# Optimization experiments

Hardware: AMD Instinct MI355X
Metric: run time of the kernel (lower is better)

## Reference

```python
import jax, jax.numpy as jnp
import numpy as np

IMG_SIZE = 416.0
CLASS_NUM = 80
NUM_ANCH = 3
MAX_GT = 64  # fixed padding for per-image valid GT boxes (original uses a variable-size python loop)


def _bce_logits(x, t):
    # BCEWithLogits, elementwise: softplus(x) - x*t  (numerically stable)
    return jax.nn.softplus(x) - x * t


def _make_noobj_mask(pred_boxes, targets):
    # pred_boxes: [B,G,G,3,4] in pixel units; targets: [B,G,G,3,85]
    B, G = pred_boxes.shape[0], pred_boxes.shape[1]
    N = G * G * NUM_ANCH
    conf = targets[..., 4].reshape(B, N)
    boxes = targets[..., 0:4].reshape(B, N, 4)
    # gather up to MAX_GT ground-truth boxes per image (conf>0 are the valid ones)
    top_conf, idx = jax.lax.top_k(conf, MAX_GT)            # [B,M]
    gt = jnp.take_along_axis(boxes, idx[..., None], axis=1)  # [B,M,4]
    valid = top_conf > 0.0                                   # [B,M]

    p = pred_boxes.reshape(B, N, 4)
    pxy = p[:, :, None, 0:2]   # [B,N,1,2]
    pwh = p[:, :, None, 2:4]
    gxy = gt[:, None, :, 0:2]  # [B,1,M,2]
    gwh = gt[:, None, :, 2:4]

    imin = jnp.maximum(pxy - pwh / 2, gxy - gwh / 2)
    imax = jnp.minimum(pxy + pwh / 2, gxy + gwh / 2)
    iwh = jnp.maximum(imax - imin, 0.0)
    inter = iwh[..., 0] * iwh[..., 1]                        # [B,N,M]
    area_p = pwh[..., 0] * pwh[..., 1]
    area_g = gwh[..., 0] * gwh[..., 1]
    iou = inter / (area_p + area_g - inter + 1e-9)
    iou = jnp.where(valid[:, None, :], iou, 0.0)
    best_iou = jnp.max(iou, axis=-1)                         # [B,N]
    noobj = (best_iou < 0.6).astype(pred_boxes.dtype)
    return noobj.reshape(B, G, G, NUM_ANCH)


def reference(preds, targets, anchors):
    B, G = preds.shape[0], preds.shape[1]
    ratio = IMG_SIZE / G
    p = preds.reshape(B, G, G, NUM_ANCH, 5 + CLASS_NUM)
    box_xy_raw, box_wh_raw, conf_logit, cls_logit = jnp.split(p, [2, 4, 5], axis=-1)

    # grid offsets: offset[i,j] = (j, i)
    gx, gy = jnp.meshgrid(jnp.arange(G, dtype=preds.dtype), jnp.arange(G, dtype=preds.dtype))
    offset = jnp.stack([gx, gy], axis=-1).reshape(G, G, 1, 2)

    sig_xy = jax.nn.sigmoid(box_xy_raw)
    box_xy = (sig_xy + offset) * ratio                 # pixel units
    box_wh = jnp.exp(box_wh_raw) * anchors             # (anchors/ratio)*ratio = anchors
    pred_boxes = jnp.concatenate([box_xy, box_wh], axis=-1)

    preds_xy = box_xy / ratio - offset                 # == sig_xy
    true_xy = targets[..., 0:2] / ratio - offset
    true_wh = targets[..., 2:4] / anchors
    preds_wh = box_wh / anchors
    true_wh = jnp.where(true_wh == 0.0, 1.0, true_wh)
    preds_wh = jnp.where(preds_wh == 0.0, 1.0, preds_wh)
    true_wh = jnp.log(jnp.clip(true_wh, 1e-9, 1e9))
    preds_wh = jnp.log(jnp.clip(preds_wh, 1e-9, 1e9))

    obj = (targets[..., 4] > 0.0).astype(preds.dtype)  # [B,G,G,3]
    obj_e = obj[..., None]
    scale = 2.0 - targets[..., 2:3] / IMG_SIZE * targets[..., 3:4] / IMG_SIZE  # [B,G,G,3,1]

    txty_loss = jnp.sum(obj_e * (preds_xy - true_xy) ** 2 * scale) / B
    twth_loss = jnp.sum(obj_e * (preds_wh - true_wh) ** 2 * scale) / B

    noobj = _make_noobj_mask(pred_boxes, targets)      # [B,G,G,3]
    noobj_conf_mask = (1.0 - obj) * noobj
    conf_t = targets[..., 4:5]
    noobj_conf_loss = jnp.sum(noobj_conf_mask[..., None] * _bce_logits(conf_logit, conf_t)) / B
    obj_conf_loss = jnp.sum(obj_e * _bce_logits(conf_logit, conf_t)) / B
    class_loss = jnp.sum(obj_e * _bce_logits(cls_logit, targets[..., 5:])) / B

    total_loss = txty_loss + twth_loss + noobj_conf_loss + obj_conf_loss + class_loss
    return (txty_loss, twth_loss, noobj_conf_loss, obj_conf_loss, class_loss, total_loss)


def setup_inputs() -> dict:
    key = jax.random.key(0)
    ks = jax.random.split(key, 5)
    B, G, A, C = 32, 52, NUM_ANCH, CLASS_NUM
    N = G * G * A
    M_OBJ = 40  # GT boxes per image (< MAX_GT)
    preds = jax.random.normal(ks[0], (B, G, G, A * (5 + C)), jnp.float32) * 0.5
    idx = jax.random.randint(ks[1], (B, M_OBJ), 0, N)
    xy = jax.random.uniform(ks[2], (B, M_OBJ, 2), jnp.float32, 0.0, IMG_SIZE)
    wh = jax.random.uniform(ks[3], (B, M_OBJ, 2), jnp.float32, 16.0, 128.0)
    cid = jax.random.randint(ks[4], (B, M_OBJ), 0, C)
    onehot = jax.nn.one_hot(cid, C, dtype=jnp.float32)
    vals = jnp.concatenate([xy, wh, jnp.ones((B, M_OBJ, 1), jnp.float32), onehot], axis=-1)
    t = jnp.zeros((B, N, 5 + C), jnp.float32)
    t = t.at[jnp.arange(B)[:, None], idx].set(vals)
    targets = t.reshape(B, G, G, A, 5 + C)
    anchors = jnp.array([[10.0, 13.0], [16.0, 30.0], [33.0, 23.0]], jnp.float32)
    return {"preds": preds, "targets": targets, "anchors": anchors}
```

## Files before the change

kernel.cpp:

```cpp
#include <hip/hip_runtime.h>
#include <math.h>

#define GSZ 52
#define NA 3
#define NCLS 80
#define CH 85
#define NCA (GSZ*GSZ*NA)
#define MAXGT 64
#define MCHUNK 32
#define CLSU 16

__device__ __forceinline__ float softplus_fast(float x) {
    return fmaxf(x, 0.0f) + __logf(1.0f + __expf(-fabsf(x)));
}

__global__ void k_init(int* cnt, int B) {
    if (threadIdx.x < B) cnt[threadIdx.x] = 0;
}

__device__ __forceinline__ void emit_gt(const float* __restrict__ tg, int glob,
                                        int* cnt, float4* __restrict__ gtbox,
                                        int2* __restrict__ gtinfo) {
    const float* r = tg + (size_t)glob * CH;
    int b    = glob / NCA;
    int nloc = glob - b * NCA;
    int cid = 0;
#pragma unroll 16
    for (int c = 0; c < NCLS; c++) if (r[5 + c] > 0.5f) cid = c;
    int pos = atomicAdd(cnt + b, 1);
    if (pos < MAXGT) {
        gtbox[b * MAXGT + pos]  = make_float4(r[0], r[1], r[2], r[3]);
        gtinfo[b * MAXGT + pos] = make_int2(nloc, cid);
    }
}

__global__ __launch_bounds__(256) void k_scan(
    const float* __restrict__ tg, const float* __restrict__ pr,
    const float* __restrict__ anchors, int nrec, int* cnt,
    float4* __restrict__ gtbox, int2* __restrict__ gtinfo,
    float4* __restrict__ boxdec, float* __restrict__ confdec) {
    int tid = threadIdx.x;
    int rec = blockIdx.x * 128 + (tid & 127);
    if (rec >= nrec) return;

    const float* rp = pr + (size_t)rec * CH;
    if (tid < 128) {
        float r0 = rp[0], r1 = rp[1], r2 = rp[2], r3 = rp[3];
        int b    = rec / NCA;
        int n    = rec - b * NCA;
        int a    = n % NA;
        int cell = n / NA;
        int gi = cell / GSZ, gj = cell % GSZ;
        float aw = anchors[2 * a], ah = anchors[2 * a + 1];
        float sx = __builtin_amdgcn_rcpf(1.0f + __expf(-r0));
        float sy = __builtin_amdgcn_rcpf(1.0f + __expf(-r1));
        float bx = (sx + (float)gj) * 8.0f;
        float by = (sy + (float)gi) * 8.0f;
        float bw = __expf(r2) * aw;
        float bh = __expf(r3) * ah;
        boxdec[rec] = make_float4(bx, by, bw, bh);
    } else {
        float pc     = rp[4];
        float conf_t = tg[(size_t)rec * CH + 4];
        confdec[rec] = pc;
        if (conf_t > 0.0f) emit_gt(tg, rec, cnt, gtbox, gtinfo);
    }
}

__global__ __launch_bounds__(256) void k_nc(
    const float* __restrict__ pr,
    const float* __restrict__ anchors,
    const int* __restrict__ cnt,
    const float4* __restrict__ gtbox,
    const int2* __restrict__ gtinfo,
    const float4* __restrict__ boxdec,
    const float* __restrict__ confdec,
    float* __restrict__ partial,
    float4* __restrict__ cls4) {
    __shared__ float4 sbox[MAXGT];
    __shared__ int    sidx[MAXGT];
    __shared__ float  swsum[4];

    int b   = blockIdx.y;
    int tid = threadIdx.x;

    if (blockIdx.x < MCHUNK) {
        int n = blockIdx.x * 256 + tid;
        int m = min(cnt[b], MAXGT);
        if (tid < m) {
            sbox[tid] = gtbox[b * MAXGT + tid];
            sidx[tid] = gtinfo[b * MAXGT + tid].x;
        }
        __syncthreads();

        float v = 0.0f;
        if (n < NCA) {
            size_t rec = (size_t)b * NCA + n;
            float4 pb = boxdec[rec];
            float  pc = confdec[rec];
            float px0 = pb.x - pb.z * 0.5f, px1 = pb.x + pb.z * 0.5f;
            float py0 = pb.y - pb.w * 0.5f, py1 = pb.y + pb.w * 0.5f;
            float areap = pb.z * pb.w;

            float best = 0.0f;
            bool isobj = false;
            for (int k = 0; k < m; k++) {
                float4 g = sbox[k];
                isobj |= (sidx[k] == n);
                float ix = fminf(px1, g.x + g.z * 0.5f) - fmaxf(px0, g.x - g.z * 0.5f);
                float iy = fminf(py1, g.y + g.w * 0.5f) - fmaxf(py0, g.y - g.w * 0.5f);
                float inter = fmaxf(ix, 0.0f) * fmaxf(iy, 0.0f);
                float u = areap + g.z * g.w - inter + 1e-9f;
                best = fmaxf(best, inter * __builtin_amdgcn_rcpf(u));
            }
            if (!isobj && best < 0.6f) v = softplus_fast(pc);
        }

        int lane = tid & 63;
        int wv   = tid >> 6;
        for (int off = 32; off > 0; off >>= 1) v += __shfl_down(v, off);
        if (lane == 0) swsum[wv] = v;
        __syncthreads();
        if (tid == 0)
            partial[b * MCHUNK + blockIdx.x] = swsum[0] + swsum[1] + swsum[2] + swsum[3];
    } else {
        int wv   = tid >> 6;
        int lane = tid & 63;
        int slot = b * MAXGT + (blockIdx.x - MCHUNK) * 4 + wv;
        int k    = slot & (MAXGT - 1);

        float4 resv = make_float4(0.f, 0.f, 0.f, 0.f);
        int m = min(cnt[b], MAXGT);
        if (k < m) {
            float4 g  = gtbox[slot];
            int2 info = gtinfo[slot];
            int n = info.x, cid = info.y;
            size_t rec = (size_t)b * NCA + n;
            const float* cl = pr + rec * CH + 5;

            float x0 = cl[lane];
            float cls = softplus_fast(x0) - (lane == cid ? x0 : 0.0f);
            if (lane < NCLS - 64) {
                float x1 = cl[64 + lane];
                cls += softplus_fast(x1) - ((64 + lane) == cid ? x1 : 0.0f);
            }
            for (int off = 32; off > 0; off >>= 1) cls += __shfl_down(cls, off);

            if (lane == 0) {
                float4 pb = boxdec[rec];
                float  pc = confdec[rec];
                int a    = n % NA;
                int cell = n / NA;
                int gi = cell / GSZ, gj = cell % GSZ;
                float aw = anchors[2 * a], ah = anchors[2 * a + 1];

                float scale = 2.0f - (g.z * (1.0f / 416.0f)) * (g.w * (1.0f / 416.0f));
                float dx = (pb.x * 0.125f - (float)gj) - (g.x * 0.125f - (float)gj);
                float dy = (pb.y * 0.125f - (float)gi) - (g.y * 0.125f - (float)gi);
                float txty = (dx * dx + dy * dy) * scale;

                float rw = __builtin_amdgcn_rcpf(aw), rh = __builtin_amdgcn_rcpf(ah);
                float pwr = fminf(fmaxf(pb.z * rw, 1e-9f), 1e9f);
                float phr = fminf(fmaxf(pb.w * rh, 1e-9f), 1e9f);
                float twr = fminf(fmaxf(g.z  * rw, 1e-9f), 1e9f);
                float thr = fminf(fmaxf(g.w  * rh, 1e-9f), 1e9f);
                float dw = __logf(pwr) - __logf(twr);
                float dh = __logf(phr) - __logf(thr);
                float twth = (dw * dw + dh * dh) * scale;

                float obj = softplus_fast(pc) - pc;
                resv = make_float4(txty, twth, obj, cls);
            }
        }
        if (lane == 0) cls4[slot] = resv;
    }
}

__global__ void k_final(const float* __restrict__ partial, int np,
                        const float4* __restrict__ cls4, int ns,
                        int B, float* __restrict__ out) {
    __shared__ double sred[4 * 5];
    int tid = threadIdx.x;
    double acc[5] = {0, 0, 0, 0, 0};
    for (int i = tid; i < np; i += 256) acc[2] += (double)partial[i];
    for (int i = tid; i < ns; i += 256) {
        float4 v = cls4[i];
        acc[0] += (double)v.x; acc[1] += (double)v.y;
        acc[3] += (double)v.z; acc[4] += (double)v.w;
    }
    int lane = tid & 63;
    int wv   = tid >> 6;
#pragma unroll
    for (int i = 0; i < 5; i++) {
        double v = acc[i];
        for (int off = 32; off > 0; off >>= 1) v += __shfl_down(v, off);
        if (lane == 0) sred[wv * 5 + i] = v;
    }
    __syncthreads();
    if (tid == 0) {
        double tot = 0.0;
#pragma unroll
        for (int i = 0; i < 5; i++) {
            double r = (sred[i] + sred[5 + i] + sred[10 + i] + sred[15 + i]) / (double)B;
            out[i] = (float)r;
            tot += r;
        }
        out[5] = (float)tot;
    }
}

extern "C" void kernel_launch(void* const* d_in, const int* in_sizes, int n_in,
                              void* d_out, int out_size, void* d_ws, size_t ws_size,
                              hipStream_t stream) {
    const float* preds   = (const float*)d_in[0];
    const float* targets = (const float*)d_in[1];
    const float* anchors = (const float*)d_in[2];
    float* out = (float*)d_out;

    int B = in_sizes[0] / (NCA * CH);
    int nrec = B * NCA;
    int scan_blocks = (nrec + 127) / 128;
    int np = MCHUNK * B;
    int ns = B * MAXGT;

    char* ws = (char*)d_ws;
    size_t off = 0;
    int*    cnt     = (int*)(ws + off);      off += 128;
    float4* gtbox   = (float4*)(ws + off);   off += (size_t)ns * sizeof(float4);
    int2*   gtinfo  = (int2*)(ws + off);     off += (size_t)ns * sizeof(int2);
    float*  partial = (float*)(ws + off);    off += (size_t)np * sizeof(float);
    off = (off + 15) & ~(size_t)15;
    float4* boxdec  = (float4*)(ws + off);   off += (size_t)nrec * sizeof(float4);
    float*  confdec = (float*)(ws + off);    off += (size_t)nrec * sizeof(float);
    off = (off + 15) & ~(size_t)15;
    float4* cls4    = (float4*)(ws + off);   off += (size_t)ns * sizeof(float4);

    k_init<<<1, 64, 0, stream>>>(cnt, B);
    k_scan<<<scan_blocks, 256, 0, stream>>>(targets, preds, anchors, nrec, cnt,
                                            gtbox, gtinfo, boxdec, confdec);
    dim3 grid(MCHUNK + CLSU, B);
    k_nc<<<grid, 256, 0, stream>>>(preds, anchors, cnt, gtbox, gtinfo,
                                   boxdec, confdec, partial, cls4);
    k_final<<<1, 256, 0, stream>>>(partial, np, cls4, ns, B, out);
}
```

Baseline: 193.1 us.

## Stage scan records through shared memory with coalesced float4 loads

The scan kernel now loads 32 full 85-float records from both targets and preds into shared memory using coalesced float4 loads across the block, then decodes boxes and extracts GT entries from LDS. Before, each thread read a few scalars at a stride of 85 floats, which gives poorly coalesced access. The trade-off is that every record's full 340 bytes are now read from both tensors, and a block barrier plus about 22 KB of LDS per block are added. It also assumes nrec divides by 32, which holds for this grid size.

```diff
diff --git a/kernel.cpp b/kernel.cpp
--- a/kernel.cpp
+++ b/kernel.cpp
@@ -7,6 +7,9 @@
 #define CH 85
 #define NCA (GSZ*GSZ*NA)
 #define MAXGT 64
+#define RPB 32
+#define FPT (RPB*CH)
+#define F4PT (FPT/4)
 #define MCHUNK 32
 #define CLSU 16
 
@@ -18,52 +21,74 @@
     if (threadIdx.x < B) cnt[threadIdx.x] = 0;
 }
 
-__device__ __forceinline__ void emit_gt(const float* __restrict__ tg, int glob,
-                                        int* cnt, float4* __restrict__ gtbox,
-                                        int2* __restrict__ gtinfo) {
-    const float* r = tg + (size_t)glob * CH;
-    int b    = glob / NCA;
-    int nloc = glob - b * NCA;
-    int cid = 0;
-#pragma unroll 16
-    for (int c = 0; c < NCLS; c++) if (r[5 + c] > 0.5f) cid = c;
-    int pos = atomicAdd(cnt + b, 1);
-    if (pos < MAXGT) {
-        gtbox[b * MAXGT + pos]  = make_float4(r[0], r[1], r[2], r[3]);
-        gtinfo[b * MAXGT + pos] = make_int2(nloc, cid);
-    }
-}
-
 __global__ __launch_bounds__(256) void k_scan(
     const float* __restrict__ tg, const float* __restrict__ pr,
-    const float* __restrict__ anchors, int nrec, int* cnt,
+    const float* __restrict__ anchors, int* cnt,
     float4* __restrict__ gtbox, int2* __restrict__ gtinfo,
     float4* __restrict__ boxdec, float* __restrict__ confdec) {
+    __shared__ float sT[FPT];
+    __shared__ float sP[FPT];
     int tid = threadIdx.x;
-    int rec = blockIdx.x * 128 + (tid & 127);
-    if (rec >= nrec) return;
-
-    const float* rp = pr + (size_t)rec * CH;
-    if (tid < 128) {
-        float r0 = rp[0], r1 = rp[1], r2 = rp[2], r3 = rp[3];
-        int b    = rec / NCA;
-        int n    = rec - b * NCA;
-        int a    = n % NA;
-        int cell = n / NA;
+    size_t rec0 = (size_t)blockIdx.x * RPB;
+
+    {
+        const float4* srcT = (const float4*)(tg + rec0 * CH);
+        const float4* srcP = (const float4*)(pr + rec0 * CH);
+        float4* dT = (float4*)sT;
+        float4* dP = (float4*)sP;
+        bool has3 = (tid < F4PT - 512);
+        float4 a0 = srcT[tid];
+        float4 b0 = srcP[tid];
+        float4 a1 = srcT[tid + 256];
+        float4 b1 = srcP[tid + 256];
+        float4 a2 = make_float4(0.f, 0.f, 0.f, 0.f);
+        float4 b2 = a2;
+        if (has3) {
+            a2 = srcT[tid + 512];
+            b2 = srcP[tid + 512];
+        }
+        dT[tid]       = a0;  dP[tid]       = b0;
+        dT[tid + 256] = a1;  dP[tid + 256] = b1;
+        if (has3) {
+            dT[tid + 512] = a2;
+            dP[tid + 512] = b2;
+        }
+    }
+    __syncthreads();
+
+    if (tid < RPB) {
+        const float* r = sT + tid * CH;
+        float conf = r[4];
+        if (conf > 0.0f) {
+            size_t glob = rec0 + tid;
+            int b    = (int)(glob / NCA);
+            int nloc = (int)(glob - (size_t)b * NCA);
+            int cid = 0;
+#pragma unroll 16
+            for (int c = 0; c < NCLS; c++) if (r[5 + c] > 0.5f) cid = c;
+            int pos = atomicAdd(cnt + b, 1);
+            if (pos < MAXGT) {
+                gtbox[b * MAXGT + pos]  = make_float4(r[0], r[1], r[2], r[3]);
+                gtinfo[b * MAXGT + pos] = make_int2(nloc, cid);
+            }
+        }
+    } else if (tid >= 64 && tid < 64 + RPB) {
+        int t = tid - 64;
+        const float* r = sP + t * CH;
+        size_t glob = rec0 + t;
+        int b    = (int)(glob / NCA);
+        int nloc = (int)(glob - (size_t)b * NCA);
+        int a    = nloc % NA;
+        int cell = nloc / NA;
         int gi = cell / GSZ, gj = cell % GSZ;
+        float sx = __builtin_amdgcn_rcpf(1.0f + __expf(-r[0]));
+        float sy = __builtin_amdgcn_rcpf(1.0f + __expf(-r[1]));
+        float ew = __expf(r[2]), eh = __expf(r[3]);
         float aw = anchors[2 * a], ah = anchors[2 * a + 1];
-        float sx = __builtin_amdgcn_rcpf(1.0f + __expf(-r0));
-        float sy = __builtin_amdgcn_rcpf(1.0f + __expf(-r1));
-        float bx = (sx + (float)gj) * 8.0f;
-        float by = (sy + (float)gi) * 8.0f;
-        float bw = __expf(r2) * aw;
-        float bh = __expf(r3) * ah;
-        boxdec[rec] = make_float4(bx, by, bw, bh);
-    } else {
-        float pc     = rp[4];
-        float conf_t = tg[(size_t)rec * CH + 4];
-        confdec[rec] = pc;
-        if (conf_t > 0.0f) emit_gt(tg, rec, cnt, gtbox, gtinfo);
+        boxdec[glob]  = make_float4((sx + (float)gj) * 8.0f,
+                                    (sy + (float)gi) * 8.0f,
+                                    ew * aw, eh * ah);
+        confdec[glob] = r[4];
     }
 }
 
@@ -219,7 +244,7 @@
 
     int B = in_sizes[0] / (NCA * CH);
     int nrec = B * NCA;
-    int scan_blocks = (nrec + 127) / 128;
+    int scan_blocks = nrec / RPB;
     int np = MCHUNK * B;
     int ns = B * MAXGT;
 
@@ -236,7 +261,7 @@
     float4* cls4    = (float4*)(ws + off);   off += (size_t)ns * sizeof(float4);
 
     k_init<<<1, 64, 0, stream>>>(cnt, B);
-    k_scan<<<scan_blocks, 256, 0, stream>>>(targets, preds, anchors, nrec, cnt,
+    k_scan<<<scan_blocks, 256, 0, stream>>>(targets, preds, anchors, cnt,
                                             gtbox, gtinfo, boxdec, confdec);
     dim3 grid(MCHUNK + CLSU, B);
     k_nc<<<grid, 256, 0, stream>>>(preds, anchors, cnt, gtbox, gtinfo,
```

After: 208.4 us. +7.9%, slower.
